# Optimization experiments

Measured on AMD Instinct MI355X. Metric: run time of the kernel, lower is better.

The kernel has to match this reference:

```python
import jax, jax.numpy as jnp
import numpy as np

B, L, D1, D2 = 4, 2048, 1024, 1024

def setup_inputs() -> dict:
    key = jax.random.key(0)
    k1, k2, k3, k4, k5, k6 = jax.random.split(key, 6)
    s1 = 1.0 / np.sqrt(D1)
    s2 = 1.0 / np.sqrt(D2)
    return {
        "features_1": jax.random.normal(k1, (B, L, D1), dtype=jnp.float32),
        "features_2": jax.random.normal(k2, (B, L, D2), dtype=jnp.float32),
        # nn.Linear(d1, d2): W1 [d2, d1], b1 [d2]
        "W1": jax.random.uniform(k3, (D2, D1), jnp.float32, -s1, s1),
        "b1": jax.random.uniform(k4, (D2,), jnp.float32, -s1, s1),
        # nn.Linear(d2, d1): W2 [d1, d2], b2 [d1]
        "W2": jax.random.uniform(k5, (D1, D2), jnp.float32, -s2, s2),
        "b2": jax.random.uniform(k6, (D1,), jnp.float32, -s2, s2),
    }

def reference(features_1, features_2, W1, b1, W2, b2):
    # transformed_features_1: [B, L, D2]
    t1 = jnp.einsum('bld,ed->ble', features_1, W1) + b1
    # unscaled similarity: [B, L, L]
    sim = jnp.einsum('ble,bme->blm', t1, features_2)
    attn = jax.nn.softmax(sim, axis=-1)  # both softmaxes are identical
    attended_1 = jnp.einsum('blm,bme->ble', attn, features_2)  # [B, L, D2]
    attended_2 = jnp.einsum('blm,bme->ble', attn, t1)          # [B, L, D2]
    attended_2 = jnp.einsum('ble,de->bld', attended_2, W2) + b2  # [B, L, D1]
    return attended_1, attended_2
```

## Files before the change

kernel.cpp:

```cpp
#include <hip/hip_runtime.h>
#include <stdint.h>

#define BB 4
#define LL 2048
#define DD 1024

typedef __attribute__((ext_vector_type(4))) float f32x4;
typedef __attribute__((ext_vector_type(8))) _Float16 f16x8;
typedef __attribute__((ext_vector_type(4))) unsigned short u16x4;
typedef unsigned short u16;

__device__ __forceinline__ u16 f2h(float x){
  return __builtin_bit_cast(u16, (_Float16)x);
}

__device__ __forceinline__ void gload16(const u16* g, u16* l){
  __builtin_amdgcn_global_load_lds((const __attribute__((address_space(1))) unsigned*)g,
                                   (__attribute__((address_space(3))) unsigned*)l,
                                   16, 0, 0);
}

__device__ __forceinline__ int xcd_swz(int bx, int nwg){
  return (bx & 7) * (nwg >> 3) + (bx >> 3);
}

__device__ __forceinline__ void stage_tile8(u16* lds, const u16* src, int ld, int wave, int lane){
  const int r0 = lane >> 3;
  const int cs = (((lane & 7) ^ r0) << 3);
  #pragma unroll
  for (int j = 0; j < 2; ++j){
    const int rb = wave*16 + j*8;
    gload16(src + (size_t)(rb + r0)*ld + cs, lds + rb*64);
  }
}

__device__ __forceinline__ f16x8 frag_ld(const u16* t, int row, int ko){
  return __builtin_bit_cast(f16x8,
    *reinterpret_cast<const f32x4*>(t + row*64 + (ko ^ ((row & 7) << 3))));
}

__global__ void cast_k(const float* __restrict__ src, u16* __restrict__ dst, int n4){
  const int stride = gridDim.x * blockDim.x;
  for (int i = blockIdx.x*blockDim.x + threadIdx.x; i < n4; i += stride){
    f32x4 v = reinterpret_cast<const f32x4*>(src)[i];
    u16x4 h;
    #pragma unroll
    for (int j = 0; j < 4; ++j) h[j] = f2h(v[j]);
    reinterpret_cast<u16x4*>(dst)[i] = h;
  }
}

template<int EPI>
__global__ __launch_bounds__(512,2) void gemm8p_k(
    const u16* __restrict__ A_g, long long sAb, int lda,
    const u16* __restrict__ B0_g, const u16* __restrict__ B1_g, long long sBb, int ldb,
    float* __restrict__ C0, float* __restrict__ C1, long long sCb, int ldc,
    const float* __restrict__ bias, int NT){
  __shared__ __align__(16) u16 As[4][128*64];
  __shared__ __align__(16) u16 Bs[4][128*64];
  const int b = blockIdx.y;
  const int bx = xcd_swz(blockIdx.x, gridDim.x);
  const int bm = bx >> 3, bn = bx & 7;
  const int tid = threadIdx.x, wave = tid>>6, lane = tid&63;
  const int wm = wave & 1, wn = wave >> 1;
  const int r0 = lane >> 3, cs = (((lane&7) ^ r0) << 3);
  const int rb0 = wave*16;
  const u16* Ab = A_g + (size_t)b*sAb + (size_t)(bm*256)*lda;
  const u16* Bb = (EPI == 0)
      ? (B0_g + (size_t)b*sBb + (size_t)(bn*256)*ldb)
      : (((bn < 4) ? B0_g : B1_g) + (size_t)b*sBb + (size_t)((bn&3)*256)*ldb);

  f32x4 acc[2][2][4][2];
  #pragma unroll
  for (int i=0;i<2;i++)
    #pragma unroll
    for (int j=0;j<2;j++)
      #pragma unroll
      for (int m=0;m<4;m++)
        #pragma unroll
        for (int n=0;n<2;n++) acc[i][j][m][n] = (f32x4){0.f,0.f,0.f,0.f};

  auto stA = [&](int tt, int h){
    const u16* s = Ab + (size_t)(h*128 + rb0 + r0)*lda + (size_t)tt*64 + cs;
    u16* d = &As[((tt&1)<<1)+h][rb0*64];
    gload16(s, d);
    gload16(s + (size_t)8*lda, d + 8*64);
  };
  auto stB = [&](int tt, int h){
    const u16* s = Bb + (size_t)(h*128 + rb0 + r0)*ldb + (size_t)tt*64 + cs;
    u16* d = &Bs[((tt&1)<<1)+h][rb0*64];
    gload16(s, d);
    gload16(s + (size_t)8*ldb, d + 8*64);
  };

  stA(0,0); stB(0,0); stA(0,1); stB(0,1);
  stA(1,0); stB(1,0);
  asm volatile("s_waitcnt vmcnt(4)" ::: "memory");
  __builtin_amdgcn_s_barrier();

  for (int t = 0; t < NT; ++t){
    #pragma unroll
    for (int p = 0; p < 4; ++p){
      const u16* Ah = As[((t&1)<<1) + (p>>1)];
      const u16* Bh = Bs[((t&1)<<1) + (p&1)];
      f16x8 af[4][2], bf[2][2];
      #pragma unroll
      for (int mi=0;mi<4;mi++)
        #pragma unroll
        for (int ks=0;ks<2;ks++)
          af[mi][ks] = frag_ld(Ah, wm*64 + mi*16 + (lane&15), ks*32 + ((lane>>4)<<3));
      #pragma unroll
      for (int ni=0;ni<2;ni++)
        #pragma unroll
        for (int ks=0;ks<2;ks++)
          bf[ni][ks] = frag_ld(Bh, wn*32 + ni*16 + (lane&15), ks*32 + ((lane>>4)<<3));
      if (p == 0){ if (t+1 < NT) stA(t+1, 1); }
      else if (p == 1){ if (t+1 < NT) stB(t+1, 1); }
      else if (p == 2){ if (t+2 < NT) stA(t+2, 0); }
      else {
        if (t+2 < NT){ stB(t+2, 0); asm volatile("s_waitcnt vmcnt(4)" ::: "memory"); }
        else         {              asm volatile("s_waitcnt vmcnt(0)" ::: "memory"); }
      }
      __builtin_amdgcn_s_barrier();
      asm volatile("s_waitcnt lgkmcnt(0)" ::: "memory");
      __builtin_amdgcn_sched_barrier(0);
      __builtin_amdgcn_s_setprio(1);
      #pragma unroll
      for (int mi=0;mi<4;mi++)
        #pragma unroll
        for (int ni=0;ni<2;ni++)
          #pragma unroll
          for (int ks=0;ks<2;ks++)
            acc[p>>1][p&1][mi][ni] = __builtin_amdgcn_mfma_f32_16x16x32_f16(
                af[mi][ks], bf[ni][ks], acc[p>>1][p&1][mi][ni], 0,0,0);
      __builtin_amdgcn_s_setprio(0);
      __builtin_amdgcn_sched_barrier(0);
      __builtin_amdgcn_s_barrier();
    }
  }

  #pragma unroll
  for (int qm=0;qm<2;qm++)
    #pragma unroll
    for (int qn=0;qn<2;qn++)
      #pragma unroll
      for (int mi=0;mi<4;mi++)
        #pragma unroll
        for (int ni=0;ni<2;ni++){
          const int r = bm*256 + qm*128 + wm*64 + mi*16 + ((lane>>4)<<2);
          if (EPI == 0){
            const int c = bn*256 + qn*128 + wn*32 + ni*16 + (lane&15);
            float* Cb = C0 + (size_t)b*sCb;
            #pragma unroll
            for (int j=0;j<4;j++)
              Cb[(size_t)(r+j)*ldc + c] = acc[qm][qn][mi][ni][j];
          } else {
            const int c = (bn&3)*256 + qn*128 + wn*32 + ni*16 + (lane&15);
            float* O = ((bn < 4) ? C0 : C1) + (size_t)b*sCb;
            const float bv = (bn >= 4) ? bias[c] : 0.f;
            #pragma unroll
            for (int j=0;j<4;j++)
              O[(size_t)(r+j)*ldc + c] = acc[qm][qn][mi][ni][j] + bv;
          }
        }
}

template<int EPI>
__global__ __launch_bounds__(512,4) void gemm_h_k(
    const u16* __restrict__ A_g, long long sAb, int lda,
    const u16* __restrict__ B_g, long long sBb, int ldb,
    float* __restrict__ C, long long sCb, int ldc,
    const float* __restrict__ bias, u16* __restrict__ Oh,
    int K, int tn_sh){
  __shared__ __align__(16) u16 As[128*64];
  __shared__ __align__(16) u16 Bs[128*64];
  const int b = blockIdx.y;
  const int bx = xcd_swz(blockIdx.x, gridDim.x);
  const int bm = bx >> tn_sh, bn = bx & ((1 << tn_sh) - 1);
  const int tid = threadIdx.x, wave = tid>>6, lane = tid&63;
  const int wr = wave>>2, wc = wave&3;
  const u16* Ab = A_g + (size_t)b*sAb + (size_t)(bm*128)*lda;
  const u16* Bb = B_g + (size_t)b*sBb + (size_t)(bn*128)*ldb;
  f32x4 acc[4][2];
  #pragma unroll
  for (int i=0;i<4;i++)
    #pragma unroll
    for (int j=0;j<2;j++) acc[i][j] = (f32x4){0.f,0.f,0.f,0.f};

  for (int k0 = 0; k0 < K; k0 += 64){
    __syncthreads();
    stage_tile8(As, Ab + k0, lda, wave, lane);
    stage_tile8(Bs, Bb + k0, ldb, wave, lane);
    __syncthreads();
    #pragma unroll
    for (int kk=0;kk<2;kk++){
      const int ko = kk*32 + ((lane>>4)<<3);
      f16x8 a[4], bb[2];
      #pragma unroll
      for (int mi=0;mi<4;mi++) a[mi]  = frag_ld(As, wr*64 + mi*16 + (lane&15), ko);
      #pragma unroll
      for (int ni=0;ni<2;ni++) bb[ni] = frag_ld(Bs, wc*32 + ni*16 + (lane&15), ko);
      #pragma unroll
      for (int mi=0;mi<4;mi++)
        #pragma unroll
        for (int ni=0;ni<2;ni++)
          acc[mi][ni] = __builtin_amdgcn_mfma_f32_16x16x32_f16(a[mi], bb[ni], acc[mi][ni], 0,0,0);
    }
  }
  const int m0 = bm*128, n0 = bn*128;
  if (EPI == 0){
    float* Cb = C + (size_t)b*sCb;
    #pragma unroll
    for (int mi=0;mi<4;mi++)
      #pragma unroll
      for (int ni=0;ni<2;ni++){
        const int r = m0 + wr*64 + mi*16 + ((lane>>4)<<2);
        const int c = n0 + wc*32 + ni*16 + (lane&15);
        #pragma unroll
        for (int j=0;j<4;j++)
          Cb[(size_t)(r+j)*ldc + c] = acc[mi][ni][j];
      }
  } else {
    #pragma unroll
    for (int mi=0;mi<4;mi++)
      #pragma unroll
      for (int ni=0;ni<2;ni++){
        const int r = m0 + wr*64 + mi*16 + ((lane>>4)<<2);
        const int c = n0 + wc*32 + ni*16 + (lane&15);
        const float bv = bias[c];
        #pragma unroll
        for (int j=0;j<4;j++)
          Oh[(size_t)(r+j)*ldc + c] = f2h(acc[mi][ni][j] + bv);
      }
  }
}

__global__ __launch_bounds__(256) void softmax_k(float* __restrict__ sim){
  const int row = blockIdx.x;
  float* p = sim + (size_t)row * LL;
  const int tid = threadIdx.x, wave = tid>>6, lane = tid&63;
  f32x4 x0 = reinterpret_cast<const f32x4*>(p)[tid];
  f32x4 x1 = reinterpret_cast<const f32x4*>(p)[tid + 256];
  float mx = fmaxf(fmaxf(fmaxf(x0[0],x0[1]), fmaxf(x0[2],x0[3])),
                   fmaxf(fmaxf(x1[0],x1[1]), fmaxf(x1[2],x1[3])));
  #pragma unroll
  for (int o = 32; o; o >>= 1) mx = fmaxf(mx, __shfl_xor(mx, o, 64));
  __shared__ float red[8];
  if (lane == 0) red[wave] = mx;
  __syncthreads();
  mx = fmaxf(fmaxf(red[0], red[1]), fmaxf(red[2], red[3]));
  float e0[4], e1[4], s = 0.f;
  #pragma unroll
  for (int j=0;j<4;j++){ e0[j] = __expf(x0[j]-mx); s += e0[j]; }
  #pragma unroll
  for (int j=0;j<4;j++){ e1[j] = __expf(x1[j]-mx); s += e1[j]; }
  #pragma unroll
  for (int o = 32; o; o >>= 1) s += __shfl_xor(s, o, 64);
  if (lane == 0) red[4+wave] = s;
  __syncthreads();
  s = (red[4]+red[5]) + (red[6]+red[7]);
  const float inv = 1.0f / s;
  u16* ob = reinterpret_cast<u16*>(p);
  u16x4 w0, w1;
  #pragma unroll
  for (int j=0;j<4;j++){ w0[j] = f2h(e0[j]*inv); w1[j] = f2h(e1[j]*inv); }
  reinterpret_cast<u16x4*>(ob)[tid]       = w0;
  reinterpret_cast<u16x4*>(ob)[tid + 256] = w1;
}

__global__ void transpose_k(const u16* __restrict__ in, u16* __restrict__ out){
  __shared__ u16 t[32][33];
  const int b = blockIdx.z;
  const int e0 = blockIdx.x*32, m0 = blockIdx.y*32;
  const u16* src = in  + (size_t)b*LL*DD;
  u16* dst       = out + (size_t)b*DD*LL;
  for (int j = threadIdx.y; j < 32; j += 8)
    t[j][threadIdx.x] = src[(size_t)(m0+j)*DD + e0 + threadIdx.x];
  __syncthreads();
  for (int j = threadIdx.y; j < 32; j += 8)
    dst[(size_t)(e0+j)*LL + m0 + threadIdx.x] = t[threadIdx.x][j];
}

__global__ __launch_bounds__(512,4) void gemm_zt_k(const u16* __restrict__ t1f,
                                                   const u16* __restrict__ w2f,
                                                   u16* __restrict__ ZT){
  __shared__ __align__(16) u16 As[128*64];
  __shared__ __align__(16) u16 Bs[128*64];
  const int bx = xcd_swz(blockIdx.x, gridDim.x);
  const int bm = bx >> 3, bn = bx & 7;
  const int tid = threadIdx.x, wave = tid>>6, lane = tid&63;
  const int wr = wave>>2, wc = wave&3;
  const u16* Ab = t1f + (size_t)(bm*128)*DD;
  const u16* Bb = w2f + (size_t)(bn*128)*DD;
  f32x4 acc[4][2];
  #pragma unroll
  for (int i=0;i<4;i++)
    #pragma unroll
    for (int j=0;j<2;j++) acc[i][j] = (f32x4){0.f,0.f,0.f,0.f};

  for (int k0 = 0; k0 < DD; k0 += 64){
    __syncthreads();
    stage_tile8(As, Ab + k0, DD, wave, lane);
    stage_tile8(Bs, Bb + k0, DD, wave, lane);
    __syncthreads();
    #pragma unroll
    for (int kk=0;kk<2;kk++){
      const int ko = kk*32 + ((lane>>4)<<3);
      f16x8 a[4], bb[2];
      #pragma unroll
      for (int mi=0;mi<4;mi++) a[mi]  = frag_ld(As, wr*64 + mi*16 + (lane&15), ko);
      #pragma unroll
      for (int ni=0;ni<2;ni++) bb[ni] = frag_ld(Bs, wc*32 + ni*16 + (lane&15), ko);
      #pragma unroll
      for (int mi=0;mi<4;mi++)
        #pragma unroll
        for (int ni=0;ni<2;ni++)
          acc[mi][ni] = __builtin_amdgcn_mfma_f32_16x16x32_f16(a[mi], bb[ni], acc[mi][ni], 0,0,0);
    }
  }
  #pragma unroll
  for (int mi=0;mi<4;mi++)
    #pragma unroll
    for (int ni=0;ni<2;ni++){
      const int l = bm*128 + wr*64 + mi*16 + ((lane>>4)<<2);
      const int b2i = l >> 11, m = l & 2047;
      const int d = bn*128 + wc*32 + ni*16 + (lane&15);
      u16x4 w;
      #pragma unroll
      for (int j=0;j<4;j++) w[j] = f2h(acc[mi][ni][j]);
      *reinterpret_cast<u16x4*>(ZT + ((size_t)b2i*DD + d)*LL + m) = w;
    }
}

extern "C" void kernel_launch(void* const* d_in, const int* in_sizes, int n_in,
                              void* d_out, int out_size, void* d_ws, size_t ws_size,
                              hipStream_t stream) {
  const float* f1 = (const float*)d_in[0];
  const float* f2 = (const float*)d_in[1];
  const float* W1 = (const float*)d_in[2];
  const float* b1 = (const float*)d_in[3];
  const float* W2 = (const float*)d_in[4];
  const float* b2 = (const float*)d_in[5];
  float* out1 = (float*)d_out;
  float* out2 = out1 + (size_t)BB*LL*DD;

  char* ws = (char*)d_ws;
  u16* t1f = (u16*)(ws + 0);
  u16* ZT  = (u16*)(ws + 16777216);
  u16* f2f = (u16*)(ws + 33554432);
  u16* f2T = (u16*)(ws + 50331648);
  u16* w1f = (u16*)(ws + 67108864);
  u16* w2f = (u16*)(ws + 69206016);
  float* sim = (float*)(ws + 71303168);
  u16* f1f = (u16*)(ws + 71303168);

  cast_k<<<4096, 256, 0, stream>>>(f2, f2f, (BB*LL*DD)/4);
  cast_k<<<4096, 256, 0, stream>>>(f1, f1f, (BB*LL*DD)/4);
  cast_k<<<1024, 256, 0, stream>>>(W1, w1f, (DD*DD)/4);
  cast_k<<<1024, 256, 0, stream>>>(W2, w2f, (DD*DD)/4);
  gemm_h_k<1><<<dim3(512, 1), 512, 0, stream>>>(f1f, 0, DD,
                                                w1f, 0, DD,
                                                nullptr, 0, DD,
                                                b1, t1f, DD, 3);
  gemm8p_k<0><<<dim3(64, BB), 512, 0, stream>>>(t1f, (long long)LL*DD, DD,
                                                f2f, nullptr, (long long)LL*DD, DD,
                                                sim, nullptr, (long long)LL*LL, LL,
                                                nullptr, 16);
  softmax_k<<<BB*LL, 256, 0, stream>>>(sim);
  transpose_k<<<dim3(32, 64, BB), dim3(32, 8), 0, stream>>>(f2f, f2T);
  gemm_zt_k<<<dim3(512, 1), 512, 0, stream>>>(t1f, w2f, ZT);
  gemm8p_k<1><<<dim3(64, BB), 512, 0, stream>>>((const u16*)sim, (long long)LL*4096, 4096,
                                                f2T, ZT, (long long)DD*LL, LL,
                                                out1, out2, (long long)LL*DD, DD,
                                                b2, 32);
}
```

Before: 213.8 us.

## Fuse casts with transpose, stage ZT transpose in LDS, use 128-tile PV GEMM

Fuses the f2 cast with its transpose into one kernel and merges the remaining three casts into a single launch, removing separate transpose and cast kernels. The ZT GEMM epilogue now transposes through an LDS buffer so it writes 16-byte contiguous stores instead of scattered 8-byte ones. The final attention-times-values GEMM moves from the pipelined 256x256 kernel to a simpler 128x128 tile kernel with more blocks. The extra LDS in the ZT kernel and losing the pipelined kernel for the largest GEMM could lower occupancy or throughput.

Measured after the change: 209.7 us. Within noise of the previous version (-1.9%).

```diff
diff --git a/kernel.cpp b/kernel.cpp
--- a/kernel.cpp
+++ b/kernel.cpp
@@ -8,6 +8,7 @@
 typedef __attribute__((ext_vector_type(4))) float f32x4;
 typedef __attribute__((ext_vector_type(8))) _Float16 f16x8;
 typedef __attribute__((ext_vector_type(4))) unsigned short u16x4;
+typedef __attribute__((ext_vector_type(8))) unsigned short u16x8;
 typedef unsigned short u16;
 
 __device__ __forceinline__ u16 f2h(float x){
@@ -39,23 +40,47 @@
     *reinterpret_cast<const f32x4*>(t + row*64 + (ko ^ ((row & 7) << 3))));
 }
 
-__global__ void cast_k(const float* __restrict__ src, u16* __restrict__ dst, int n4){
+__global__ void cast3_k(const float* __restrict__ f1, u16* __restrict__ f1f,
+                        const float* __restrict__ W1, u16* __restrict__ w1f,
+                        const float* __restrict__ W2, u16* __restrict__ w2f){
+  const int n1 = (BB*LL*DD)/4, nw = (DD*DD)/4;
   const int stride = gridDim.x * blockDim.x;
-  for (int i = blockIdx.x*blockDim.x + threadIdx.x; i < n4; i += stride){
-    f32x4 v = reinterpret_cast<const f32x4*>(src)[i];
+  for (int i = blockIdx.x*blockDim.x + threadIdx.x; i < n1 + 2*nw; i += stride){
+    const float* s; u16* d; int k;
+    if (i < n1){ s = f1; d = f1f; k = i; }
+    else if (i < n1 + nw){ s = W1; d = w1f; k = i - n1; }
+    else { s = W2; d = w2f; k = i - n1 - nw; }
+    f32x4 v = reinterpret_cast<const f32x4*>(s)[k];
     u16x4 h;
     #pragma unroll
     for (int j = 0; j < 4; ++j) h[j] = f2h(v[j]);
-    reinterpret_cast<u16x4*>(dst)[i] = h;
-  }
-}
-
-template<int EPI>
+    reinterpret_cast<u16x4*>(d)[k] = h;
+  }
+}
+
+__global__ void castT_k(const float* __restrict__ f2, u16* __restrict__ f2f,
+                        u16* __restrict__ f2T){
+  __shared__ u16 t[32][33];
+  const int b = blockIdx.z;
+  const int d0 = blockIdx.x*32, l0 = blockIdx.y*32;
+  const float* src = f2 + (size_t)b*LL*DD;
+  u16* d1 = f2f + (size_t)b*LL*DD;
+  u16* d2 = f2T + (size_t)b*DD*LL;
+  const int x = threadIdx.x;
+  for (int j = threadIdx.y; j < 32; j += 8){
+    u16 h = f2h(src[(size_t)(l0+j)*DD + d0 + x]);
+    d1[(size_t)(l0+j)*DD + d0 + x] = h;
+    t[j][x] = h;
+  }
+  __syncthreads();
+  for (int j = threadIdx.y; j < 32; j += 8)
+    d2[(size_t)(d0+j)*LL + l0 + x] = t[x][j];
+}
+
 __global__ __launch_bounds__(512,2) void gemm8p_k(
     const u16* __restrict__ A_g, long long sAb, int lda,
-    const u16* __restrict__ B0_g, const u16* __restrict__ B1_g, long long sBb, int ldb,
-    float* __restrict__ C0, float* __restrict__ C1, long long sCb, int ldc,
-    const float* __restrict__ bias, int NT){
+    const u16* __restrict__ B_g, long long sBb, int ldb,
+    float* __restrict__ C, long long sCb, int ldc, int NT){
   __shared__ __align__(16) u16 As[4][128*64];
   __shared__ __align__(16) u16 Bs[4][128*64];
   const int b = blockIdx.y;
@@ -66,9 +91,7 @@
   const int r0 = lane >> 3, cs = (((lane&7) ^ r0) << 3);
   const int rb0 = wave*16;
   const u16* Ab = A_g + (size_t)b*sAb + (size_t)(bm*256)*lda;
-  const u16* Bb = (EPI == 0)
-      ? (B0_g + (size_t)b*sBb + (size_t)(bn*256)*ldb)
-      : (((bn < 4) ? B0_g : B1_g) + (size_t)b*sBb + (size_t)((bn&3)*256)*ldb);
+  const u16* Bb = B_g + (size_t)b*sBb + (size_t)(bn*256)*ldb;
 
   f32x4 acc[2][2][4][2];
   #pragma unroll
@@ -148,49 +171,35 @@
         #pragma unroll
         for (int ni=0;ni<2;ni++){
           const int r = bm*256 + qm*128 + wm*64 + mi*16 + ((lane>>4)<<2);
-          if (EPI == 0){
-            const int c = bn*256 + qn*128 + wn*32 + ni*16 + (lane&15);
-            float* Cb = C0 + (size_t)b*sCb;
-            #pragma unroll
-            for (int j=0;j<4;j++)
-              Cb[(size_t)(r+j)*ldc + c] = acc[qm][qn][mi][ni][j];
-          } else {
-            const int c = (bn&3)*256 + qn*128 + wn*32 + ni*16 + (lane&15);
-            float* O = ((bn < 4) ? C0 : C1) + (size_t)b*sCb;
-            const float bv = (bn >= 4) ? bias[c] : 0.f;
-            #pragma unroll
-            for (int j=0;j<4;j++)
-              O[(size_t)(r+j)*ldc + c] = acc[qm][qn][mi][ni][j] + bv;
-          }
+          const int c = bn*256 + qn*128 + wn*32 + ni*16 + (lane&15);
+          float* Cb = C + (size_t)b*sCb;
+          #pragma unroll
+          for (int j=0;j<4;j++)
+            Cb[(size_t)(r+j)*ldc + c] = acc[qm][qn][mi][ni][j];
         }
 }
 
-template<int EPI>
-__global__ __launch_bounds__(512,4) void gemm_h_k(
-    const u16* __restrict__ A_g, long long sAb, int lda,
-    const u16* __restrict__ B_g, long long sBb, int ldb,
-    float* __restrict__ C, long long sCb, int ldc,
-    const float* __restrict__ bias, u16* __restrict__ Oh,
-    int K, int tn_sh){
+__global__ __launch_bounds__(512,4) void gemm_t1_k(
+    const u16* __restrict__ A_g, const u16* __restrict__ B_g,
+    const float* __restrict__ bias, u16* __restrict__ Oh){
   __shared__ __align__(16) u16 As[128*64];
   __shared__ __align__(16) u16 Bs[128*64];
-  const int b = blockIdx.y;
   const int bx = xcd_swz(blockIdx.x, gridDim.x);
-  const int bm = bx >> tn_sh, bn = bx & ((1 << tn_sh) - 1);
+  const int bm = bx >> 3, bn = bx & 7;
   const int tid = threadIdx.x, wave = tid>>6, lane = tid&63;
   const int wr = wave>>2, wc = wave&3;
-  const u16* Ab = A_g + (size_t)b*sAb + (size_t)(bm*128)*lda;
-  const u16* Bb = B_g + (size_t)b*sBb + (size_t)(bn*128)*ldb;
+  const u16* Ab = A_g + (size_t)(bm*128)*DD;
+  const u16* Bb = B_g + (size_t)(bn*128)*DD;
   f32x4 acc[4][2];
   #pragma unroll
   for (int i=0;i<4;i++)
     #pragma unroll
     for (int j=0;j<2;j++) acc[i][j] = (f32x4){0.f,0.f,0.f,0.f};
 
-  for (int k0 = 0; k0 < K; k0 += 64){
-    __syncthreads();
-    stage_tile8(As, Ab + k0, lda, wave, lane);
-    stage_tile8(Bs, Bb + k0, ldb, wave, lane);
+  for (int k0 = 0; k0 < DD; k0 += 64){
+    __syncthreads();
+    stage_tile8(As, Ab + k0, DD, wave, lane);
+    stage_tile8(Bs, Bb + k0, DD, wave, lane);
     __syncthreads();
     #pragma unroll
     for (int kk=0;kk<2;kk++){
@@ -207,32 +216,17 @@
           acc[mi][ni] = __builtin_amdgcn_mfma_f32_16x16x32_f16(a[mi], bb[ni], acc[mi][ni], 0,0,0);
     }
   }
-  const int m0 = bm*128, n0 = bn*128;
-  if (EPI == 0){
-    float* Cb = C + (size_t)b*sCb;
-    #pragma unroll
-    for (int mi=0;mi<4;mi++)
-      #pragma unroll
-      for (int ni=0;ni<2;ni++){
-        const int r = m0 + wr*64 + mi*16 + ((lane>>4)<<2);
-        const int c = n0 + wc*32 + ni*16 + (lane&15);
-        #pragma unroll
-        for (int j=0;j<4;j++)
-          Cb[(size_t)(r+j)*ldc + c] = acc[mi][ni][j];
-      }
-  } else {
-    #pragma unroll
-    for (int mi=0;mi<4;mi++)
-      #pragma unroll
-      for (int ni=0;ni<2;ni++){
-        const int r = m0 + wr*64 + mi*16 + ((lane>>4)<<2);
-        const int c = n0 + wc*32 + ni*16 + (lane&15);
-        const float bv = bias[c];
-        #pragma unroll
-        for (int j=0;j<4;j++)
-          Oh[(size_t)(r+j)*ldc + c] = f2h(acc[mi][ni][j] + bv);
-      }
-  }
+  #pragma unroll
+  for (int mi=0;mi<4;mi++)
+    #pragma unroll
+    for (int ni=0;ni<2;ni++){
+      const int r = bm*128 + wr*64 + mi*16 + ((lane>>4)<<2);
+      const int c = bn*128 + wc*32 + ni*16 + (lane&15);
+      const float bv = bias[c];
+      #pragma unroll
+      for (int j=0;j<4;j++)
+        Oh[(size_t)(r+j)*DD + c] = f2h(acc[mi][ni][j] + bv);
+    }
 }
 
 __global__ __launch_bounds__(256) void softmax_k(float* __restrict__ sim){
@@ -268,24 +262,12 @@
   reinterpret_cast<u16x4*>(ob)[tid + 256] = w1;
 }
 
-__global__ void transpose_k(const u16* __restrict__ in, u16* __restrict__ out){
-  __shared__ u16 t[32][33];
-  const int b = blockIdx.z;
-  const int e0 = blockIdx.x*32, m0 = blockIdx.y*32;
-  const u16* src = in  + (size_t)b*LL*DD;
-  u16* dst       = out + (size_t)b*DD*LL;
-  for (int j = threadIdx.y; j < 32; j += 8)
-    t[j][threadIdx.x] = src[(size_t)(m0+j)*DD + e0 + threadIdx.x];
-  __syncthreads();
-  for (int j = threadIdx.y; j < 32; j += 8)
-    dst[(size_t)(e0+j)*LL + m0 + threadIdx.x] = t[threadIdx.x][j];
-}
-
 __global__ __launch_bounds__(512,4) void gemm_zt_k(const u16* __restrict__ t1f,
                                                    const u16* __restrict__ w2f,
                                                    u16* __restrict__ ZT){
   __shared__ __align__(16) u16 As[128*64];
   __shared__ __align__(16) u16 Bs[128*64];
+  __shared__ u16 T[128*132];
   const int bx = xcd_swz(blockIdx.x, gridDim.x);
   const int bm = bx >> 3, bn = bx & 7;
   const int tid = threadIdx.x, wave = tid>>6, lane = tid&63;
@@ -322,13 +304,81 @@
   for (int mi=0;mi<4;mi++)
     #pragma unroll
     for (int ni=0;ni<2;ni++){
-      const int l = bm*128 + wr*64 + mi*16 + ((lane>>4)<<2);
-      const int b2i = l >> 11, m = l & 2047;
-      const int d = bn*128 + wc*32 + ni*16 + (lane&15);
-      u16x4 w;
-      #pragma unroll
-      for (int j=0;j<4;j++) w[j] = f2h(acc[mi][ni][j]);
-      *reinterpret_cast<u16x4*>(ZT + ((size_t)b2i*DD + d)*LL + m) = w;
+      const int r = wr*64 + mi*16 + ((lane>>4)<<2);
+      const int c = wc*32 + ni*16 + (lane&15);
+      #pragma unroll
+      for (int j=0;j<4;j++)
+        T[(r+j)*132 + c] = f2h(acc[mi][ni][j]);
+    }
+  __syncthreads();
+  const int b2i = bm >> 4;
+  const int mb  = (bm*128) & 2047;
+  const int d   = tid >> 2, m0 = (tid & 3) << 5;
+  u16* dst = ZT + ((size_t)b2i*DD + bn*128 + d)*LL + mb + m0;
+  #pragma unroll
+  for (int g = 0; g < 4; ++g){
+    u16x8 v;
+    #pragma unroll
+    for (int e = 0; e < 8; ++e) v[e] = T[(m0 + g*8 + e)*132 + d];
+    *reinterpret_cast<u16x8*>(dst + g*8) = v;
+  }
+}
+
+__global__ __launch_bounds__(512,4) void gemm_pv_k(const u16* __restrict__ attn,
+                                                   const u16* __restrict__ f2T,
+                                                   const u16* __restrict__ ZT,
+                                                   float* __restrict__ out1,
+                                                   float* __restrict__ out2,
+                                                   const float* __restrict__ b2){
+  __shared__ __align__(16) u16 As[128*64];
+  __shared__ __align__(16) u16 Bs[128*64];
+  const int b = blockIdx.y;
+  const int bx = xcd_swz(blockIdx.x, gridDim.x);
+  const int bm = bx >> 4, bn = bx & 15;
+  const int tid = threadIdx.x, wave = tid>>6, lane = tid&63;
+  const int wr = wave>>2, wc = wave&3;
+  const u16* Ab = attn + (size_t)b*LL*4096 + (size_t)(bm*128)*4096;
+  const u16* Bbase = (bn < 8) ? f2T : ZT;
+  const int d0 = (bn & 7) * 128;
+  const u16* Bb = Bbase + (size_t)b*DD*LL + (size_t)d0*LL;
+  f32x4 acc[4][2];
+  #pragma unroll
+  for (int i=0;i<4;i++)
+    #pragma unroll
+    for (int j=0;j<2;j++) acc[i][j] = (f32x4){0.f,0.f,0.f,0.f};
+
+  for (int k0 = 0; k0 < LL; k0 += 64){
+    __syncthreads();
+    stage_tile8(As, Ab + k0, 4096, wave, lane);
+    stage_tile8(Bs, Bb + k0, LL, wave, lane);
+    __syncthreads();
+    #pragma unroll
+    for (int kk=0;kk<2;kk++){
+      const int ko = kk*32 + ((lane>>4)<<3);
+      f16x8 a[4], bb[2];
+      #pragma unroll
+      for (int mi=0;mi<4;mi++) a[mi]  = frag_ld(As, wr*64 + mi*16 + (lane&15), ko);
+      #pragma unroll
+      for (int ni=0;ni<2;ni++) bb[ni] = frag_ld(Bs, wc*32 + ni*16 + (lane&15), ko);
+      #pragma unroll
+      for (int mi=0;mi<4;mi++)
+        #pragma unroll
+        for (int ni=0;ni<2;ni++)
+          acc[mi][ni] = __builtin_amdgcn_mfma_f32_16x16x32_f16(a[mi], bb[ni], acc[mi][ni], 0,0,0);
+    }
+  }
+  float* O = ((bn < 8) ? out1 : out2) + (size_t)b*LL*DD;
+  const bool has_bias = (bn >= 8);
+  #pragma unroll
+  for (int mi=0;mi<4;mi++)
+    #pragma unroll
+    for (int ni=0;ni<2;ni++){
+      const int r = bm*128 + wr*64 + mi*16 + ((lane>>4)<<2);
+      const int c = d0 + wc*32 + ni*16 + (lane&15);
+      const float bv = has_bias ? b2[c] : 0.f;
+      #pragma unroll
+      for (int j=0;j<4;j++)
+        O[(size_t)(r+j)*DD + c] = acc[mi][ni][j] + bv;
     }
 }
 
@@ -354,23 +404,14 @@
   float* sim = (float*)(ws + 71303168);
   u16* f1f = (u16*)(ws + 71303168);
 
-  cast_k<<<4096, 256, 0, stream>>>(f2, f2f, (BB*LL*DD)/4);
-  cast_k<<<4096, 256, 0, stream>>>(f1, f1f, (BB*LL*DD)/4);
-  cast_k<<<1024, 256, 0, stream>>>(W1, w1f, (DD*DD)/4);
-  cast_k<<<1024, 256, 0, stream>>>(W2, w2f, (DD*DD)/4);
-  gemm_h_k<1><<<dim3(512, 1), 512, 0, stream>>>(f1f, 0, DD,
-                                                w1f, 0, DD,
-                                                nullptr, 0, DD,
-                                                b1, t1f, DD, 3);
-  gemm8p_k<0><<<dim3(64, BB), 512, 0, stream>>>(t1f, (long long)LL*DD, DD,
-                                                f2f, nullptr, (long long)LL*DD, DD,
-                                                sim, nullptr, (long long)LL*LL, LL,
-                                                nullptr, 16);
+  castT_k<<<dim3(32, 64, BB), dim3(32, 8), 0, stream>>>(f2, f2f, f2T);
+  cast3_k<<<4096, 256, 0, stream>>>(f1, f1f, W1, w1f, W2, w2f);
+  gemm_t1_k<<<dim3(512, 1), 512, 0, stream>>>(f1f, w1f, b1, t1f);
+  gemm8p_k<<<dim3(64, BB), 512, 0, stream>>>(t1f, (long long)LL*DD, DD,
+                                             f2f, (long long)LL*DD, DD,
+                                             sim, (long long)LL*LL, LL, 16);
   softmax_k<<<BB*LL, 256, 0, stream>>>(sim);
-  transpose_k<<<dim3(32, 64, BB), dim3(32, 8), 0, stream>>>(f2f, f2T);
   gemm_zt_k<<<dim3(512, 1), 512, 0, stream>>>(t1f, w2f, ZT);
-  gemm8p_k<1><<<dim3(64, BB), 512, 0, stream>>>((const u16*)sim, (long long)LL*4096, 4096,
-                                                f2T, ZT, (long long)DD*LL, LL,
-                                                out1, out2, (long long)LL*DD, DD,
-                                                b2, 32);
-}
+  gemm_pv_k<<<dim3(256, BB), 512, 0, stream>>>((const u16*)sim, f2T, ZT,
+                                               out1, out2, b2);
+}
```
